# Kernel tuning notes

Measured on AMD Instinct MI355X. Metric: run time of the kernel, lower is better.

Reference implementation:

```python
import jax, jax.numpy as jnp
import numpy as np

N_NODES = 100000
N_EDGES = 1200000
F_IN, F_HID, F_OUT = 64, 16, 40


def setup_inputs() -> dict:
    key = jax.random.key(0)
    ks = jax.random.split(key, 6)
    x = jax.random.normal(ks[0], (N_NODES, F_IN), dtype=jnp.float32)
    edge_index = jax.random.randint(ks[1], (2, N_EDGES), 0, N_NODES, dtype=jnp.int32)
    s1 = 1.0 / np.sqrt(F_IN)
    s2 = 1.0 / np.sqrt(F_HID)
    return {
        "x": x,
        "edge_index": edge_index,
        "W1_self": jax.random.normal(ks[2], (F_IN, F_HID), dtype=jnp.float32) * s1,
        "W1_neigh": jax.random.normal(ks[3], (F_IN, F_HID), dtype=jnp.float32) * s1,
        "b1": jnp.zeros((F_HID,), dtype=jnp.float32),
        "W2_self": jax.random.normal(ks[4], (F_HID, F_OUT), dtype=jnp.float32) * s2,
        "W2_neigh": jax.random.normal(ks[5], (F_HID, F_OUT), dtype=jnp.float32) * s2,
        "b2": jnp.zeros((F_OUT,), dtype=jnp.float32),
    }


def _sage_conv(x, src, dst, W_self, W_neigh, b):
    # gather source features along edges, mean-aggregate onto destinations
    n = x.shape[0]
    deg = jax.ops.segment_sum(jnp.ones((src.shape[0],), x.dtype), dst, num_segments=n)
    agg = jax.ops.segment_sum(x[src], dst, num_segments=n)
    agg = agg / jnp.maximum(deg, 1.0)[:, None]
    return x @ W_self + agg @ W_neigh + b


def reference(x, edge_index, W1_self, W1_neigh, b1, W2_self, W2_neigh, b2):
    src, dst = edge_index[0], edge_index[1]
    h = jax.nn.relu(_sage_conv(x, src, dst, W1_self, W1_neigh, b1))
    # F.dropout with training=False is identity (eval-mode reference)
    out = _sage_conv(h, src, dst, W2_self, W2_neigh, b2)
    return jax.nn.log_softmax(out, axis=1)
```

## Files before the change

### kernel.cpp

```cpp
#include <hip/hip_runtime.h>
#include <math.h>

#define N_NODES 100000
#define N_EDGES 1200000
#define F_IN    64
#define F_HID   16
#define F_OUT   40

#define BK_SHIFT 7
#define BK_NODES 128
#define NB 782
#define CAP 2048
#define CAP_SHIFT 11
#define SEG_CAP 24
#define PADB 512
#define S1_EPB 4096
#define BIN_BLOCKS 293
#define N_TILES ((N_NODES + 15) / 16)
#define GEMM_BLOCKS ((N_TILES + 7) / 8)

typedef _Float16 v4h  __attribute__((ext_vector_type(4)));
typedef _Float16 v8hf __attribute__((ext_vector_type(8)));
typedef float    vf4  __attribute__((ext_vector_type(4)));

__global__ __launch_bounds__(256)
void k1_bin_gemm(const int* __restrict__ src, const int* __restrict__ dst,
                 unsigned short* __restrict__ cnt_t, unsigned* __restrict__ region,
                 const float* __restrict__ x, const float* __restrict__ Wn,
                 const float* __restrict__ Ws, const float* __restrict__ b1,
                 _Float16* __restrict__ t1, _Float16* __restrict__ xs, int nE) {
    __shared__ unsigned cnt[NB];
    int tid = threadIdx.x;
    int bid = blockIdx.x;
    if (bid < BIN_BLOCKS) {
        for (int i = tid; i < NB; i += 256) cnt[i] = 0u;
        __syncthreads();
        int tb = bid * S1_EPB + tid * 16;
        unsigned rbase = (unsigned)bid * NB;
        if (tb + 16 <= nE) {
            const int4* d4 = (const int4*)(dst + tb);
            const int4* s4 = (const int4*)(src + tb);
#pragma unroll
            for (int j = 0; j < 4; j++) {
                int4 dv = d4[j];
                int4 sv = s4[j];
                int da[4] = {dv.x, dv.y, dv.z, dv.w};
                int sa[4] = {sv.x, sv.y, sv.z, sv.w};
#pragma unroll
                for (int q = 0; q < 4; q++) {
                    unsigned d = (unsigned)da[q];
                    unsigned b = d >> BK_SHIFT;
                    unsigned pos = atomicAdd(&cnt[b], 1u);
                    if (pos < SEG_CAP)
                        region[(rbase + b) * SEG_CAP + pos] =
                            (((unsigned)sa[q]) << BK_SHIFT) | (d & (BK_NODES - 1));
                }
            }
        } else {
            for (int e = tb; e < nE && e < tb + 16; e++) {
                unsigned d = (unsigned)dst[e];
                unsigned b = d >> BK_SHIFT;
                unsigned pos = atomicAdd(&cnt[b], 1u);
                if (pos < SEG_CAP)
                    region[(rbase + b) * SEG_CAP + pos] =
                        (((unsigned)src[e]) << BK_SHIFT) | (d & (BK_NODES - 1));
            }
        }
        __syncthreads();
        for (int i = tid; i < NB; i += 256) {
            unsigned c = cnt[i];
            cnt_t[i * PADB + bid] = (unsigned short)(c < SEG_CAP ? c : SEG_CAP);
        }
    } else {
        int wv = tid >> 6;
        int lane = tid & 63;
        int mrow = lane & 15;
        int quad = lane >> 4;
        int col = mrow;
        v8hf bn0, bn1, bs0, bs1;
#pragma unroll
        for (int j = 0; j < 8; j++) {
            int k0 = quad * 8 + j;
            bn0[j] = (_Float16)Wn[k0 * F_HID + col];
            bs0[j] = (_Float16)Ws[k0 * F_HID + col];
            bn1[j] = (_Float16)Wn[(k0 + 32) * F_HID + col];
            bs1[j] = (_Float16)Ws[(k0 + 32) * F_HID + col];
        }
        float bias = b1[col];
        int gw = (bid - BIN_BLOCKS) * 4 + wv;
#pragma unroll
        for (int t = 0; t < 2; t++) {
            int tile = gw * 2 + t;
            if (tile >= N_TILES) break;
            int row0 = tile * 16;
            const float* xr = x + (size_t)(row0 + mrow) * F_IN;
            float4 x0 = *(const float4*)(xr + quad * 8);
            float4 x1 = *(const float4*)(xr + quad * 8 + 4);
            float4 x2 = *(const float4*)(xr + 32 + quad * 8);
            float4 x3 = *(const float4*)(xr + 32 + quad * 8 + 4);
            v8hf a0, a1;
            a0[0] = (_Float16)x0.x; a0[1] = (_Float16)x0.y;
            a0[2] = (_Float16)x0.z; a0[3] = (_Float16)x0.w;
            a0[4] = (_Float16)x1.x; a0[5] = (_Float16)x1.y;
            a0[6] = (_Float16)x1.z; a0[7] = (_Float16)x1.w;
            a1[0] = (_Float16)x2.x; a1[1] = (_Float16)x2.y;
            a1[2] = (_Float16)x2.z; a1[3] = (_Float16)x2.w;
            a1[4] = (_Float16)x3.x; a1[5] = (_Float16)x3.y;
            a1[6] = (_Float16)x3.z; a1[7] = (_Float16)x3.w;
            vf4 accn = {0.f, 0.f, 0.f, 0.f};
            vf4 accs = {bias, bias, bias, bias};
            accn = __builtin_amdgcn_mfma_f32_16x16x32_f16(a0, bn0, accn, 0, 0, 0);
            accn = __builtin_amdgcn_mfma_f32_16x16x32_f16(a1, bn1, accn, 0, 0, 0);
            accs = __builtin_amdgcn_mfma_f32_16x16x32_f16(a0, bs0, accs, 0, 0, 0);
            accs = __builtin_amdgcn_mfma_f32_16x16x32_f16(a1, bs1, accs, 0, 0, 0);
#pragma unroll
            for (int r = 0; r < 4; r++) {
                int row = row0 + quad * 4 + r;
                t1[row * F_HID + col] = (_Float16)accn[r];
                xs[row * F_HID + col] = (_Float16)accs[r];
            }
        }
    }
}

__global__ __launch_bounds__(512)
void k2_sort_agg1(const unsigned short* __restrict__ cnt_t, const unsigned* __restrict__ region,
                  unsigned* __restrict__ csr, unsigned* __restrict__ node_info,
                  const _Float16* __restrict__ t1, _Float16* __restrict__ xsh) {
    __shared__ unsigned scnt[PADB];
    __shared__ unsigned segbase[BIN_BLOCKS];
    __shared__ unsigned words[CAP];
    __shared__ unsigned sorted[CAP];
    __shared__ unsigned hist[BK_NODES];
    __shared__ unsigned lcur[BK_NODES];
    __shared__ unsigned begs[BK_NODES];
    int tid = threadIdx.x;
    int b = blockIdx.x;

    unsigned myc = (tid < BIN_BLOCKS) ? (unsigned)cnt_t[b * PADB + tid] : 0u;
    scnt[tid] = myc;
    __syncthreads();
    for (int d = 1; d < PADB; d <<= 1) {
        unsigned t = (tid >= d) ? scnt[tid - d] : 0u;
        __syncthreads();
        scnt[tid] += t;
        __syncthreads();
    }
    if (tid < BIN_BLOCKS) segbase[tid] = scnt[tid] - myc;
    __syncthreads();
    unsigned count = scnt[BIN_BLOCKS - 1];
    if (count > CAP) count = CAP;

    int hw = tid >> 5, lane = tid & 31;
    for (int j = hw; j < BIN_BLOCKS; j += 16) {
        unsigned base = segbase[j];
        unsigned c = scnt[j] - base;
        if ((unsigned)lane < c) {
            unsigned pos = base + lane;
            if (pos < CAP)
                words[pos] = region[((unsigned)j * NB + b) * SEG_CAP + lane];
        }
    }
    if (tid < BK_NODES) hist[tid] = 0u;
    __syncthreads();

    for (unsigned i = tid; i < count; i += 512)
        atomicAdd(&hist[words[i] & (BK_NODES - 1)], 1u);
    __syncthreads();
    unsigned hv = (tid < BK_NODES) ? hist[tid] : 0u;
    __syncthreads();
    for (int d = 1; d < BK_NODES; d <<= 1) {
        unsigned t = (tid < BK_NODES && tid >= d) ? hist[tid - d] : 0u;
        __syncthreads();
        if (tid < BK_NODES) hist[tid] += t;
        __syncthreads();
    }
    if (tid < BK_NODES) {
        unsigned excl = hist[tid] - hv;
        begs[tid] = excl;
        lcur[tid] = excl;
        int node = (b << BK_SHIFT) + tid;
        if (node < N_NODES) node_info[node] = (excl << 16) | hv;
    }
    __syncthreads();
    for (unsigned i = tid; i < count; i += 512) {
        unsigned w = words[i];
        unsigned pos = atomicAdd(&lcur[w & (BK_NODES - 1)], 1u);
        sorted[pos] = w >> BK_SHIFT;
    }
    __syncthreads();
    unsigned* reg = csr + ((size_t)b << CAP_SHIFT);
    for (unsigned i = tid; i < count; i += 512) reg[i] = sorted[i];

    int grp = tid >> 2;
    int f = tid & 3;
    int node = (b << BK_SHIFT) + grp;
    if (node >= N_NODES) return;
    unsigned beg = begs[grp];
    unsigned end = lcur[grp];
    const v4h* t4 = (const v4h*)t1;
    float a0 = 0.f, a1 = 0.f, a2 = 0.f, a3 = 0.f;
    unsigned e = beg;
    for (; e + 8 <= end; e += 8) {
        unsigned s0 = sorted[e],     s1 = sorted[e + 1];
        unsigned s2 = sorted[e + 2], s3 = sorted[e + 3];
        unsigned s4 = sorted[e + 4], s5 = sorted[e + 5];
        unsigned s6 = sorted[e + 6], s7 = sorted[e + 7];
        v4h v0 = t4[s0 * 4 + f], v1 = t4[s1 * 4 + f];
        v4h v2 = t4[s2 * 4 + f], v3 = t4[s3 * 4 + f];
        v4h v4 = t4[s4 * 4 + f], v5 = t4[s5 * 4 + f];
        v4h v6 = t4[s6 * 4 + f], v7 = t4[s7 * 4 + f];
        a0 += (float)v0[0] + (float)v1[0] + (float)v2[0] + (float)v3[0]
            + (float)v4[0] + (float)v5[0] + (float)v6[0] + (float)v7[0];
        a1 += (float)v0[1] + (float)v1[1] + (float)v2[1] + (float)v3[1]
            + (float)v4[1] + (float)v5[1] + (float)v6[1] + (float)v7[1];
        a2 += (float)v0[2] + (float)v1[2] + (float)v2[2] + (float)v3[2]
            + (float)v4[2] + (float)v5[2] + (float)v6[2] + (float)v7[2];
        a3 += (float)v0[3] + (float)v1[3] + (float)v2[3] + (float)v3[3]
            + (float)v4[3] + (float)v5[3] + (float)v6[3] + (float)v7[3];
    }
    for (; e + 4 <= end; e += 4) {
        unsigned s0 = sorted[e],     s1 = sorted[e + 1];
        unsigned s2 = sorted[e + 2], s3 = sorted[e + 3];
        v4h v0 = t4[s0 * 4 + f], v1 = t4[s1 * 4 + f];
        v4h v2 = t4[s2 * 4 + f], v3 = t4[s3 * 4 + f];
        a0 += (float)v0[0] + (float)v1[0] + (float)v2[0] + (float)v3[0];
        a1 += (float)v0[1] + (float)v1[1] + (float)v2[1] + (float)v3[1];
        a2 += (float)v0[2] + (float)v1[2] + (float)v2[2] + (float)v3[2];
        a3 += (float)v0[3] + (float)v1[3] + (float)v2[3] + (float)v3[3];
    }
    for (; e < end; e++) {
        v4h v = t4[sorted[e] * 4 + f];
        a0 += (float)v[0]; a1 += (float)v[1]; a2 += (float)v[2]; a3 += (float)v[3];
    }
    float inv = 1.0f / fmaxf((float)(end - beg), 1.0f);
    v4h* x4 = (v4h*)xsh;
    v4h xv = x4[node * 4 + f];
    v4h hv4;
    hv4[0] = (_Float16)fmaxf((float)xv[0] + a0 * inv, 0.f);
    hv4[1] = (_Float16)fmaxf((float)xv[1] + a1 * inv, 0.f);
    hv4[2] = (_Float16)fmaxf((float)xv[2] + a2 * inv, 0.f);
    hv4[3] = (_Float16)fmaxf((float)xv[3] + a3 * inv, 0.f);
    x4[node * 4 + f] = hv4;
}

__global__ __launch_bounds__(256)
void agg2_kernel(const unsigned* __restrict__ node_info, const unsigned* __restrict__ csr,
                 const _Float16* __restrict__ h,
                 const float* __restrict__ Ws, const float* __restrict__ Wn,
                 const float* __restrict__ b2, float* __restrict__ out, int n) {
    __shared__ float sWs[F_HID * F_OUT];
    __shared__ float sWn[F_HID * F_OUT];
    __shared__ float sb[F_OUT];
    int tid = threadIdx.x;
    for (int i = tid; i < F_HID * F_OUT; i += 256) { sWs[i] = Ws[i]; sWn[i] = Wn[i]; }
    if (tid < F_OUT) sb[tid] = b2[tid];
    __syncthreads();
    int g = blockIdx.x * 256 + tid;
    int node = g >> 2;
    int f = g & 3;
    if (node >= n) return;
    unsigned info = node_info[node];
    int beg = ((node >> BK_SHIFT) << CAP_SHIFT) + (int)(info >> 16);
    int cnt = (int)(info & 0xFFFFu);
    int end = beg + cnt;
    const v4h* h4 = (const v4h*)h;
    float a0 = 0.f, a1 = 0.f, a2 = 0.f, a3 = 0.f;
    int e = beg;
    for (; e + 8 <= end; e += 8) {
        unsigned s0 = csr[e],     s1 = csr[e + 1];
        unsigned s2 = csr[e + 2], s3 = csr[e + 3];
        unsigned s4 = csr[e + 4], s5 = csr[e + 5];
        unsigned s6 = csr[e + 6], s7 = csr[e + 7];
        v4h v0 = h4[s0 * 4 + f], v1 = h4[s1 * 4 + f];
        v4h v2 = h4[s2 * 4 + f], v3 = h4[s3 * 4 + f];
        v4h v4 = h4[s4 * 4 + f], v5 = h4[s5 * 4 + f];
        v4h v6 = h4[s6 * 4 + f], v7 = h4[s7 * 4 + f];
        a0 += (float)v0[0] + (float)v1[0] + (float)v2[0] + (float)v3[0]
            + (float)v4[0] + (float)v5[0] + (float)v6[0] + (float)v7[0];
        a1 += (float)v0[1] + (float)v1[1] + (float)v2[1] + (float)v3[1]
            + (float)v4[1] + (float)v5[1] + (float)v6[1] + (float)v7[1];
        a2 += (float)v0[2] + (float)v1[2] + (float)v2[2] + (float)v3[2]
            + (float)v4[2] + (float)v5[2] + (float)v6[2] + (float)v7[2];
        a3 += (float)v0[3] + (float)v1[3] + (float)v2[3] + (float)v3[3]
            + (float)v4[3] + (float)v5[3] + (float)v6[3] + (float)v7[3];
    }
    for (; e + 4 <= end; e += 4) {
        unsigned s0 = csr[e],     s1 = csr[e + 1];
        unsigned s2 = csr[e + 2], s3 = csr[e + 3];
        v4h v0 = h4[s0 * 4 + f], v1 = h4[s1 * 4 + f];
        v4h v2 = h4[s2 * 4 + f], v3 = h4[s3 * 4 + f];
        a0 += (float)v0[0] + (float)v1[0] + (float)v2[0] + (float)v3[0];
        a1 += (float)v0[1] + (float)v1[1] + (float)v2[1] + (float)v3[1];
        a2 += (float)v0[2] + (float)v1[2] + (float)v2[2] + (float)v3[2];
        a3 += (float)v0[3] + (float)v1[3] + (float)v2[3] + (float)v3[3];
    }
    for (; e < end; e++) {
        v4h v = h4[csr[e] * 4 + f];
        a0 += (float)v[0]; a1 += (float)v[1]; a2 += (float)v[2]; a3 += (float)v[3];
    }
    float inv = 1.0f / fmaxf((float)cnt, 1.0f);
    a0 *= inv; a1 *= inv; a2 *= inv; a3 *= inv;
    v4h hs = h4[node * 4 + f];
    float h0 = (float)hs[0], h1 = (float)hs[1], h2 = (float)hs[2], h3 = (float)hs[3];
    float arow[F_HID], hrow[F_HID];
#pragma unroll
    for (int k = 0; k < 4; k++) {
        arow[4 * k + 0] = __shfl(a0, k, 4);
        arow[4 * k + 1] = __shfl(a1, k, 4);
        arow[4 * k + 2] = __shfl(a2, k, 4);
        arow[4 * k + 3] = __shfl(a3, k, 4);
        hrow[4 * k + 0] = __shfl(h0, k, 4);
        hrow[4 * k + 1] = __shfl(h1, k, 4);
        hrow[4 * k + 2] = __shfl(h2, k, 4);
        hrow[4 * k + 3] = __shfl(h3, k, 4);
    }
    float logit[10];
    float m = -INFINITY;
#pragma unroll
    for (int j = 0; j < 10; j++) {
        int c = f * 10 + j;
        float s = sb[c];
#pragma unroll
        for (int k = 0; k < F_HID; k++)
            s += hrow[k] * sWs[k * F_OUT + c] + arow[k] * sWn[k * F_OUT + c];
        logit[j] = s;
        m = fmaxf(m, s);
    }
    m = fmaxf(m, __shfl_xor(m, 1, 4));
    m = fmaxf(m, __shfl_xor(m, 2, 4));
    float sum = 0.f;
#pragma unroll
    for (int j = 0; j < 10; j++) sum += __expf(logit[j] - m);
    sum += __shfl_xor(sum, 1, 4);
    sum += __shfl_xor(sum, 2, 4);
    float lse = m + __logf(sum);
#pragma unroll
    for (int j = 0; j < 10; j++)
        out[node * F_OUT + f * 10 + j] = logit[j] - lse;
}

extern "C" void kernel_launch(void* const* d_in, const int* in_sizes, int n_in,
                              void* d_out, int out_size, void* d_ws, size_t ws_size,
                              hipStream_t stream) {
    const float* x        = (const float*)d_in[0];
    const int*   edges    = (const int*)d_in[1];
    const float* W1_self  = (const float*)d_in[2];
    const float* W1_neigh = (const float*)d_in[3];
    const float* b1       = (const float*)d_in[4];
    const float* W2_self  = (const float*)d_in[5];
    const float* W2_neigh = (const float*)d_in[6];
    const float* b2       = (const float*)d_in[7];
    float* out = (float*)d_out;

    const int* src = edges;
    const int* dst = edges + N_EDGES;

    char* base = (char*)d_ws;
    unsigned short* cnt_t    = (unsigned short*)base;
    unsigned*       node_info= (unsigned*)(base + (1u << 20));
    unsigned*       csr      = (unsigned*)(base + (2u << 20));
    unsigned*       region   = (unsigned*)(base + (16u << 20));
    _Float16*       t1       = (_Float16*)(base + (40u << 20));
    _Float16*       xsh      = (_Float16*)(base + (44u << 20));

    k1_bin_gemm<<<BIN_BLOCKS + GEMM_BLOCKS, 256, 0, stream>>>(
        src, dst, cnt_t, region, x, W1_neigh, W1_self, b1, t1, xsh, N_EDGES);
    k2_sort_agg1<<<NB, 512, 0, stream>>>(cnt_t, region, csr, node_info, t1, xsh);
    agg2_kernel<<<(N_NODES * 4 + 255) / 256, 256, 0, stream>>>(node_info, csr, xsh,
                                                               W2_self, W2_neigh, b2, out, N_NODES);
}
```

Before: 154.5 us.

## Counting-sort edges per bin block in shared memory and write contiguous region

The binning stage now builds a histogram of destination buckets, prefix-sums it, scatters edges into a shared-memory sorted array and writes that array out contiguously. Before, each edge went to a fixed 24-slot segment per bucket, which scattered writes and silently dropped overflowing edges. A packed start/count word per bucket lets the sort stage read variable-length contiguous runs. This removes the SEG_CAP truncation and gives coalesced global writes, at the cost of an extra histogram pass, a block scan and more shared memory in k1.

```diff
diff --git a/kernel.cpp b/kernel.cpp
--- a/kernel.cpp
+++ b/kernel.cpp
@@ -10,11 +10,12 @@
 #define BK_SHIFT 7
 #define BK_NODES 128
 #define NB 782
+#define NBP 1024
 #define CAP 2048
 #define CAP_SHIFT 11
-#define SEG_CAP 24
 #define PADB 512
 #define S1_EPB 4096
+#define S1_SHIFT 12
 #define BIN_BLOCKS 293
 #define N_TILES ((N_NODES + 15) / 16)
 #define GEMM_BLOCKS ((N_TILES + 7) / 8)
@@ -25,52 +26,87 @@
 
 __global__ __launch_bounds__(256)
 void k1_bin_gemm(const int* __restrict__ src, const int* __restrict__ dst,
-                 unsigned short* __restrict__ cnt_t, unsigned* __restrict__ region,
+                 unsigned* __restrict__ info_t, unsigned* __restrict__ region,
                  const float* __restrict__ x, const float* __restrict__ Wn,
                  const float* __restrict__ Ws, const float* __restrict__ b1,
                  _Float16* __restrict__ t1, _Float16* __restrict__ xs, int nE) {
-    __shared__ unsigned cnt[NB];
+    __shared__ __align__(16) char smem[21504];
     int tid = threadIdx.x;
     int bid = blockIdx.x;
     if (bid < BIN_BLOCKS) {
-        for (int i = tid; i < NB; i += 256) cnt[i] = 0u;
+        unsigned* sorted = (unsigned*)smem;
+        unsigned* hist   = (unsigned*)(smem + 16384);
+        unsigned* tsum   = (unsigned*)(smem + 20480);
+        for (int i = tid; i < NBP; i += 256) hist[i] = 0u;
         __syncthreads();
         int tb = bid * S1_EPB + tid * 16;
-        unsigned rbase = (unsigned)bid * NB;
-        if (tb + 16 <= nE) {
+        int4 dv[4], sv[4];
+        bool full = (tb + 16 <= nE);
+        if (full) {
             const int4* d4 = (const int4*)(dst + tb);
             const int4* s4 = (const int4*)(src + tb);
 #pragma unroll
+            for (int j = 0; j < 4; j++) { dv[j] = d4[j]; sv[j] = s4[j]; }
+#pragma unroll
             for (int j = 0; j < 4; j++) {
-                int4 dv = d4[j];
-                int4 sv = s4[j];
-                int da[4] = {dv.x, dv.y, dv.z, dv.w};
-                int sa[4] = {sv.x, sv.y, sv.z, sv.w};
+                atomicAdd(&hist[((unsigned)dv[j].x) >> BK_SHIFT], 1u);
+                atomicAdd(&hist[((unsigned)dv[j].y) >> BK_SHIFT], 1u);
+                atomicAdd(&hist[((unsigned)dv[j].z) >> BK_SHIFT], 1u);
+                atomicAdd(&hist[((unsigned)dv[j].w) >> BK_SHIFT], 1u);
+            }
+        } else {
+            for (int e = tb; e < nE && e < tb + 16; e++)
+                atomicAdd(&hist[((unsigned)dst[e]) >> BK_SHIFT], 1u);
+        }
+        __syncthreads();
+        unsigned c0 = hist[4 * tid], c1 = hist[4 * tid + 1];
+        unsigned c2 = hist[4 * tid + 2], c3 = hist[4 * tid + 3];
+        unsigned s = c0 + c1 + c2 + c3;
+        tsum[tid] = s;
+        __syncthreads();
+        for (int d = 1; d < 256; d <<= 1) {
+            unsigned t = (tid >= d) ? tsum[tid - d] : 0u;
+            __syncthreads();
+            tsum[tid] += t;
+            __syncthreads();
+        }
+        unsigned ex = tsum[tid] - s;
+        hist[4 * tid]     = ex;
+        hist[4 * tid + 1] = ex + c0;
+        hist[4 * tid + 2] = ex + c0 + c1;
+        hist[4 * tid + 3] = ex + c0 + c1 + c2;
+        __syncthreads();
+        {
+            unsigned st0 = hist[4 * tid];
+            if (4 * tid     < NB) info_t[(4 * tid)     * PADB + bid] = (st0 << 16) | c0;
+            if (4 * tid + 1 < NB) info_t[(4 * tid + 1) * PADB + bid] = ((st0 + c0) << 16) | c1;
+            if (4 * tid + 2 < NB) info_t[(4 * tid + 2) * PADB + bid] = ((st0 + c0 + c1) << 16) | c2;
+            if (4 * tid + 3 < NB) info_t[(4 * tid + 3) * PADB + bid] = ((st0 + c0 + c1 + c2) << 16) | c3;
+        }
+        if (full) {
+#pragma unroll
+            for (int j = 0; j < 4; j++) {
+                int da[4] = {dv[j].x, dv[j].y, dv[j].z, dv[j].w};
+                int sa[4] = {sv[j].x, sv[j].y, sv[j].z, sv[j].w};
 #pragma unroll
                 for (int q = 0; q < 4; q++) {
                     unsigned d = (unsigned)da[q];
                     unsigned b = d >> BK_SHIFT;
-                    unsigned pos = atomicAdd(&cnt[b], 1u);
-                    if (pos < SEG_CAP)
-                        region[(rbase + b) * SEG_CAP + pos] =
-                            (((unsigned)sa[q]) << BK_SHIFT) | (d & (BK_NODES - 1));
+                    unsigned pos = atomicAdd(&hist[b], 1u);
+                    sorted[pos] = (((unsigned)sa[q]) << BK_SHIFT) | (d & (BK_NODES - 1));
                 }
             }
         } else {
             for (int e = tb; e < nE && e < tb + 16; e++) {
                 unsigned d = (unsigned)dst[e];
                 unsigned b = d >> BK_SHIFT;
-                unsigned pos = atomicAdd(&cnt[b], 1u);
-                if (pos < SEG_CAP)
-                    region[(rbase + b) * SEG_CAP + pos] =
-                        (((unsigned)src[e]) << BK_SHIFT) | (d & (BK_NODES - 1));
+                unsigned pos = atomicAdd(&hist[b], 1u);
+                sorted[pos] = (((unsigned)src[e]) << BK_SHIFT) | (d & (BK_NODES - 1));
             }
         }
         __syncthreads();
-        for (int i = tid; i < NB; i += 256) {
-            unsigned c = cnt[i];
-            cnt_t[i * PADB + bid] = (unsigned short)(c < SEG_CAP ? c : SEG_CAP);
-        }
+        unsigned* reg = region + ((unsigned)bid << S1_SHIFT);
+        for (int i = tid; i < S1_EPB; i += 256) reg[i] = sorted[i];
     } else {
         int wv = tid >> 6;
         int lane = tid & 63;
@@ -124,11 +160,11 @@
 }
 
 __global__ __launch_bounds__(512)
-void k2_sort_agg1(const unsigned short* __restrict__ cnt_t, const unsigned* __restrict__ region,
+void k2_sort_agg1(const unsigned* __restrict__ info_t, const unsigned* __restrict__ region,
                   unsigned* __restrict__ csr, unsigned* __restrict__ node_info,
                   const _Float16* __restrict__ t1, _Float16* __restrict__ xsh) {
     __shared__ unsigned scnt[PADB];
-    __shared__ unsigned segbase[BIN_BLOCKS];
+    __shared__ unsigned sstart[PADB];
     __shared__ unsigned words[CAP];
     __shared__ unsigned sorted[CAP];
     __shared__ unsigned hist[BK_NODES];
@@ -137,8 +173,10 @@
     int tid = threadIdx.x;
     int b = blockIdx.x;
 
-    unsigned myc = (tid < BIN_BLOCKS) ? (unsigned)cnt_t[b * PADB + tid] : 0u;
+    unsigned info = (tid < BIN_BLOCKS) ? info_t[b * PADB + tid] : 0u;
+    unsigned myc = info & 0xFFFFu;
     scnt[tid] = myc;
+    sstart[tid] = info >> 16;
     __syncthreads();
     for (int d = 1; d < PADB; d <<= 1) {
         unsigned t = (tid >= d) ? scnt[tid - d] : 0u;
@@ -146,19 +184,18 @@
         scnt[tid] += t;
         __syncthreads();
     }
-    if (tid < BIN_BLOCKS) segbase[tid] = scnt[tid] - myc;
-    __syncthreads();
-    unsigned count = scnt[BIN_BLOCKS - 1];
+    unsigned count = scnt[PADB - 1];
     if (count > CAP) count = CAP;
 
     int hw = tid >> 5, lane = tid & 31;
     for (int j = hw; j < BIN_BLOCKS; j += 16) {
-        unsigned base = segbase[j];
-        unsigned c = scnt[j] - base;
-        if ((unsigned)lane < c) {
-            unsigned pos = base + lane;
-            if (pos < CAP)
-                words[pos] = region[((unsigned)j * NB + b) * SEG_CAP + lane];
+        unsigned tot = scnt[j];
+        unsigned c = (j == 0) ? tot : tot - scnt[j - 1];
+        unsigned wb = tot - c;
+        unsigned rb = ((unsigned)j << S1_SHIFT) + sstart[j];
+        for (unsigned off = lane; off < c; off += 32) {
+            unsigned pos = wb + off;
+            if (pos < CAP) words[pos] = region[rb + off];
         }
     }
     if (tid < BK_NODES) hist[tid] = 0u;
@@ -357,16 +394,16 @@
     const int* dst = edges + N_EDGES;
 
     char* base = (char*)d_ws;
-    unsigned short* cnt_t    = (unsigned short*)base;
-    unsigned*       node_info= (unsigned*)(base + (1u << 20));
-    unsigned*       csr      = (unsigned*)(base + (2u << 20));
-    unsigned*       region   = (unsigned*)(base + (16u << 20));
-    _Float16*       t1       = (_Float16*)(base + (40u << 20));
-    _Float16*       xsh      = (_Float16*)(base + (44u << 20));
+    unsigned* info_t    = (unsigned*)base;
+    unsigned* node_info = (unsigned*)(base + (2u << 20));
+    unsigned* csr       = (unsigned*)(base + (3u << 20));
+    unsigned* region    = (unsigned*)(base + (10u << 20));
+    _Float16* t1        = (_Float16*)(base + (16u << 20));
+    _Float16* xsh       = (_Float16*)(base + (20u << 20));
 
     k1_bin_gemm<<<BIN_BLOCKS + GEMM_BLOCKS, 256, 0, stream>>>(
-        src, dst, cnt_t, region, x, W1_neigh, W1_self, b1, t1, xsh, N_EDGES);
-    k2_sort_agg1<<<NB, 512, 0, stream>>>(cnt_t, region, csr, node_info, t1, xsh);
+        src, dst, info_t, region, x, W1_neigh, W1_self, b1, t1, xsh, N_EDGES);
+    k2_sort_agg1<<<NB, 512, 0, stream>>>(info_t, region, csr, node_info, t1, xsh);
     agg2_kernel<<<(N_NODES * 4 + 255) / 256, 256, 0, stream>>>(node_info, csr, xsh,
                                                                W2_self, W2_neigh, b2, out, N_NODES);
 }
```

Measured after the change: 144.8 us. 6.3% less time.
